# Kernel optimization log

Hardware: AMD Instinct MI355X
Metric: run time of the kernel (lower is better)

Reference implementation:

```python
import jax, jax.numpy as jnp
import numpy as np

N_H_NODES = 100000
N_G_NODES = 100000
N_EDGES = 1000000
N_GRAPHS = 64
N_H, N_G, N_X, N_U = 64, 64, 8, 16
IN_DIM = N_H + N_G + N_X + N_U  # 152
N_X_OUT = 1


def setup_inputs() -> dict:
    key = jax.random.key(0)
    ks = jax.random.split(key, 10)
    return {
        "x_h": jax.random.normal(ks[0], (N_H_NODES, N_H), dtype=jnp.float32),
        "x_g": jax.random.normal(ks[1], (N_G_NODES, N_G), dtype=jnp.float32),
        "edge_attr": jax.random.normal(ks[2], (N_EDGES, N_X), dtype=jnp.float32),
        "u": jax.random.normal(ks[3], (N_GRAPHS, N_U), dtype=jnp.float32),
        "edge_index": jax.random.randint(ks[4], (2, N_EDGES), 0, N_H_NODES, dtype=jnp.int64),
        "batch_e": jax.random.randint(ks[5], (N_EDGES,), 0, N_GRAPHS, dtype=jnp.int64),
        "W1": jax.random.normal(ks[6], (IN_DIM, N_X_OUT), dtype=jnp.float32) * 0.08,
        "b1": jnp.zeros((N_X_OUT,), dtype=jnp.float32),
        "W2": jax.random.normal(ks[7], (N_X_OUT, N_X_OUT), dtype=jnp.float32) * 0.5,
        "b2": jnp.zeros((N_X_OUT,), dtype=jnp.float32),
    }


def reference(x_h, x_g, edge_attr, u, edge_index, batch_e, W1, b1, W2, b2):
    src = edge_index[0]
    tgt = edge_index[1]
    # gather node/global features per edge and concat: [E, n_h+n_g+n_x+n_u]
    feat = jnp.concatenate([x_h[src], x_g[tgt], edge_attr, u[batch_e]], axis=1)
    h = feat @ W1 + b1                       # [E, 1]
    h = jnp.where(h >= 0, h, 0.1 * h)        # LeakyReLU(0.1)
    out = h @ W2 + b2                        # [E, 1]
    return out
```

## Files before the change

kernel.cpp:

```cpp
#include <hip/hip_runtime.h>
#include <hip/hip_bf16.h>


__global__ void node_partial_dot(const float* __restrict__ xh,
                                 const float* __restrict__ xg,
                                 const float* __restrict__ W1,
                                 float* __restrict__ ph,
                                 float* __restrict__ pg,
                                 int nh, int ng) {
    int gid  = blockIdx.x * blockDim.x + threadIdx.x;
    int wave = gid >> 6;
    int lane = gid & 63;
    int row  = wave * 4 + (lane >> 4);
    int q    = lane & 15;
    int total = nh + ng;
    if (row >= total) return;

    const float* src;
    const float* w;
    if (row < nh) { src = xh + (size_t)row * 64;        w = W1; }
    else          { src = xg + (size_t)(row - nh) * 64; w = W1 + 64; }

    float4 v  = reinterpret_cast<const float4*>(src)[q];
    float4 wv = reinterpret_cast<const float4*>(w)[q];
    float s = v.x * wv.x + v.y * wv.y + v.z * wv.z + v.w * wv.w;

    s += __shfl_xor(s, 1);
    s += __shfl_xor(s, 2);
    s += __shfl_xor(s, 4);
    s += __shfl_xor(s, 8);

    if (q == 0) {
        if (row < nh) ph[row] = s;
        else          pg[row - nh] = s;
    }
}

__global__ void edge_kernel(const int* __restrict__ edge_index,
                            const int* __restrict__ batch_e,
                            const float* __restrict__ edge_attr,
                            const float* __restrict__ u,
                            const float* __restrict__ W1,
                            const float* __restrict__ b1,
                            const float* __restrict__ W2,
                            const float* __restrict__ b2,
                            const float* __restrict__ ph,
                            const float* __restrict__ pg,
                            float* __restrict__ out,
                            int E) {
    int e = blockIdx.x * blockDim.x + threadIdx.x;
    if (e >= E) return;

    int s = edge_index[e];
    int t = edge_index[E + e];
    int g = batch_e[e];

    float h = ph[s] + pg[t] + b1[0];

    const float4* ea = reinterpret_cast<const float4*>(edge_attr + (size_t)e * 8);
    float4 a0 = ea[0], a1 = ea[1];
    const float* wx = W1 + 128;
    h += a0.x * wx[0] + a0.y * wx[1] + a0.z * wx[2] + a0.w * wx[3]
       + a1.x * wx[4] + a1.y * wx[5] + a1.z * wx[6] + a1.w * wx[7];

    const float4* ug  = reinterpret_cast<const float4*>(u + (size_t)g * 16);
    const float4* wu4 = reinterpret_cast<const float4*>(W1 + 136);
#pragma unroll
    for (int j = 0; j < 4; ++j) {
        float4 uv = ug[j];
        float4 wv = wu4[j];
        h += uv.x * wv.x + uv.y * wv.y + uv.z * wv.z + uv.w * wv.w;
    }

    h = (h >= 0.0f) ? h : 0.1f * h;
    out[e] = h * W2[0] + b2[0];
}

__global__ void edge_fallback(const int* __restrict__ edge_index,
                              const int* __restrict__ batch_e,
                              const float* __restrict__ xh,
                              const float* __restrict__ xg,
                              const float* __restrict__ edge_attr,
                              const float* __restrict__ u,
                              const float* __restrict__ W1,
                              const float* __restrict__ b1,
                              const float* __restrict__ W2,
                              const float* __restrict__ b2,
                              float* __restrict__ out,
                              int E) {
    int e = blockIdx.x * blockDim.x + threadIdx.x;
    if (e >= E) return;
    int s = edge_index[e];
    int t = edge_index[E + e];
    int g = batch_e[e];
    float h = b1[0];
    const float* hs = xh + (size_t)s * 64;
    const float* gt = xg + (size_t)t * 64;
#pragma unroll 8
    for (int j = 0; j < 64; ++j) h += hs[j] * W1[j];
#pragma unroll 8
    for (int j = 0; j < 64; ++j) h += gt[j] * W1[64 + j];
    const float* ea = edge_attr + (size_t)e * 8;
#pragma unroll
    for (int j = 0; j < 8; ++j) h += ea[j] * W1[128 + j];
    const float* ug = u + (size_t)g * 16;
#pragma unroll
    for (int j = 0; j < 16; ++j) h += ug[j] * W1[136 + j];
    h = (h >= 0.0f) ? h : 0.1f * h;
    out[e] = h * W2[0] + b2[0];
}

extern "C" void kernel_launch(void* const* d_in, const int* in_sizes, int n_in,
                              void* d_out, int out_size, void* d_ws, size_t ws_size,
                              hipStream_t stream) {
    const float* x_h       = (const float*)d_in[0];
    const float* x_g       = (const float*)d_in[1];
    const float* edge_attr = (const float*)d_in[2];
    const float* u         = (const float*)d_in[3];
    const int*   edge_idx  = (const int*)d_in[4];
    const int*   batch_e   = (const int*)d_in[5];
    const float* W1        = (const float*)d_in[6];
    const float* b1        = (const float*)d_in[7];
    const float* W2        = (const float*)d_in[8];
    const float* b2        = (const float*)d_in[9];
    float* out = (float*)d_out;

    const int E  = in_sizes[5];
    const int nh = in_sizes[0] / 64;
    const int ng = in_sizes[1] / 64;

    size_t need = (size_t)(nh + ng) * sizeof(float);
    if (ws_size >= need) {
        float* ph = (float*)d_ws;
        float* pg = ph + nh;
        int totalRows = nh + ng;
        int rowsPerBlock = 16;
        int nb = (totalRows + rowsPerBlock - 1) / rowsPerBlock;
        node_partial_dot<<<nb, 256, 0, stream>>>(x_h, x_g, W1, ph, pg, nh, ng);

        int eb = (E + 255) / 256;
        edge_kernel<<<eb, 256, 0, stream>>>(edge_idx, batch_e, edge_attr, u,
                                            W1, b1, W2, b2, ph, pg, out, E);
    } else {
        int eb = (E + 255) / 256;
        edge_fallback<<<eb, 256, 0, stream>>>(edge_idx, batch_e, x_h, x_g, edge_attr, u,
                                              W1, b1, W2, b2, out, E);
    }
}
```

Before: 31.11 us.

## Precompute per-graph u·W1 partials and process four edges per thread

The node precompute kernel also computes u[g]·W1 plus b1 for each graph, so the edge kernel gathers one scalar per edge instead of a 16-float row of u. The edge kernel now handles four edges per thread, using int4 index loads, eight float4 loads of edge_attr, and one float4 store. This cuts per-edge gather traffic and raises memory-level parallelism. In exchange there are fewer threads in flight and higher register use per thread.

After: 31.77 us. 2.1% more time.

```diff
diff --git a/kernel.cpp b/kernel.cpp
--- a/kernel.cpp
+++ b/kernel.cpp
@@ -2,78 +2,111 @@
 #include <hip/hip_bf16.h>
 
 
-__global__ void node_partial_dot(const float* __restrict__ xh,
-                                 const float* __restrict__ xg,
-                                 const float* __restrict__ W1,
-                                 float* __restrict__ ph,
-                                 float* __restrict__ pg,
-                                 int nh, int ng) {
-    int gid  = blockIdx.x * blockDim.x + threadIdx.x;
-    int wave = gid >> 6;
-    int lane = gid & 63;
-    int row  = wave * 4 + (lane >> 4);
-    int q    = lane & 15;
-    int total = nh + ng;
+__global__ void precompute_partials(const float* __restrict__ xh,
+                                    const float* __restrict__ xg,
+                                    const float* __restrict__ u,
+                                    const float* __restrict__ W1,
+                                    const float* __restrict__ b1,
+                                    float* __restrict__ ph,
+                                    float* __restrict__ pg,
+                                    float* __restrict__ pu,
+                                    int nh, int ng, int ngr) {
+    int gid = blockIdx.x * blockDim.x + threadIdx.x;
+    int row = gid >> 4;
+    int q   = gid & 15;
+    int total = nh + ng + ngr;
     if (row >= total) return;
 
-    const float* src;
-    const float* w;
-    if (row < nh) { src = xh + (size_t)row * 64;        w = W1; }
-    else          { src = xg + (size_t)(row - nh) * 64; w = W1 + 64; }
-
-    float4 v  = reinterpret_cast<const float4*>(src)[q];
-    float4 wv = reinterpret_cast<const float4*>(w)[q];
-    float s = v.x * wv.x + v.y * wv.y + v.z * wv.z + v.w * wv.w;
-
-    s += __shfl_xor(s, 1);
-    s += __shfl_xor(s, 2);
-    s += __shfl_xor(s, 4);
-    s += __shfl_xor(s, 8);
-
-    if (q == 0) {
-        if (row < nh) ph[row] = s;
-        else          pg[row - nh] = s;
+    if (row < nh + ng) {
+        const float* src = (row < nh) ? xh + (size_t)row * 64
+                                      : xg + (size_t)(row - nh) * 64;
+        const float* w   = (row < nh) ? W1 : W1 + 64;
+        float4 v  = reinterpret_cast<const float4*>(src)[q];
+        float4 wv = reinterpret_cast<const float4*>(w)[q];
+        float s = v.x * wv.x + v.y * wv.y + v.z * wv.z + v.w * wv.w;
+        s += __shfl_xor(s, 1);
+        s += __shfl_xor(s, 2);
+        s += __shfl_xor(s, 4);
+        s += __shfl_xor(s, 8);
+        if (q == 0) {
+            if (row < nh) ph[row] = s;
+            else          pg[row - nh] = s;
+        }
+    } else {
+        int g = row - nh - ng;
+        float s = 0.0f;
+        if (q < 4) {
+            float4 v  = reinterpret_cast<const float4*>(u + (size_t)g * 16)[q];
+            float4 wv = reinterpret_cast<const float4*>(W1 + 136)[q];
+            s = v.x * wv.x + v.y * wv.y + v.z * wv.z + v.w * wv.w;
+        }
+        s += __shfl_xor(s, 1);
+        s += __shfl_xor(s, 2);
+        if (q == 0) pu[g] = s + b1[0];
     }
 }
 
-__global__ void edge_kernel(const int* __restrict__ edge_index,
-                            const int* __restrict__ batch_e,
-                            const float* __restrict__ edge_attr,
-                            const float* __restrict__ u,
-                            const float* __restrict__ W1,
-                            const float* __restrict__ b1,
-                            const float* __restrict__ W2,
-                            const float* __restrict__ b2,
-                            const float* __restrict__ ph,
-                            const float* __restrict__ pg,
-                            float* __restrict__ out,
-                            int E) {
-    int e = blockIdx.x * blockDim.x + threadIdx.x;
-    if (e >= E) return;
+__global__ void edge_kernel4(const int* __restrict__ edge_index,
+                             const int* __restrict__ batch_e,
+                             const float* __restrict__ edge_attr,
+                             const float* __restrict__ W1,
+                             const float* __restrict__ W2,
+                             const float* __restrict__ b2,
+                             const float* __restrict__ ph,
+                             const float* __restrict__ pg,
+                             const float* __restrict__ pu,
+                             float* __restrict__ out,
+                             int E) {
+    int t = blockIdx.x * blockDim.x + threadIdx.x;
+    int base = t * 4;
+    if (base >= E) return;
 
-    int s = edge_index[e];
-    int t = edge_index[E + e];
-    int g = batch_e[e];
+    const float* wx = W1 + 128;
+    float w0 = wx[0], w1 = wx[1], w2 = wx[2], w3 = wx[3];
+    float w4 = wx[4], w5 = wx[5], w6 = wx[6], w7 = wx[7];
+    float w2s = W2[0], b2s = b2[0];
 
-    float h = ph[s] + pg[t] + b1[0];
+    if (base + 3 < E) {
+        int4 sv = *reinterpret_cast<const int4*>(edge_index + base);
+        int4 tv = *reinterpret_cast<const int4*>(edge_index + E + base);
+        int4 gv = *reinterpret_cast<const int4*>(batch_e + base);
 
-    const float4* ea = reinterpret_cast<const float4*>(edge_attr + (size_t)e * 8);
-    float4 a0 = ea[0], a1 = ea[1];
-    const float* wx = W1 + 128;
-    h += a0.x * wx[0] + a0.y * wx[1] + a0.z * wx[2] + a0.w * wx[3]
-       + a1.x * wx[4] + a1.y * wx[5] + a1.z * wx[6] + a1.w * wx[7];
+        const float4* eap = reinterpret_cast<const float4*>(edge_attr + (size_t)base * 8);
+        float4 ea[8];
+#pragma unroll
+        for (int j = 0; j < 8; ++j) ea[j] = eap[j];
 
-    const float4* ug  = reinterpret_cast<const float4*>(u + (size_t)g * 16);
-    const float4* wu4 = reinterpret_cast<const float4*>(W1 + 136);
+        float p0 = ph[sv.x], p1 = ph[sv.y], p2 = ph[sv.z], p3 = ph[sv.w];
+        float q0 = pg[tv.x], q1 = pg[tv.y], q2 = pg[tv.z], q3 = pg[tv.w];
+        float r0 = pu[gv.x], r1 = pu[gv.y], r2 = pu[gv.z], r3 = pu[gv.w];
+
+        float hv[4];
+        float pp[4] = {p0, p1, p2, p3};
+        float qq[4] = {q0, q1, q2, q3};
+        float rr[4] = {r0, r1, r2, r3};
 #pragma unroll
-    for (int j = 0; j < 4; ++j) {
-        float4 uv = ug[j];
-        float4 wv = wu4[j];
-        h += uv.x * wv.x + uv.y * wv.y + uv.z * wv.z + uv.w * wv.w;
+        for (int i = 0; i < 4; ++i) {
+            float4 a0 = ea[2 * i], a1 = ea[2 * i + 1];
+            float h = pp[i] + qq[i] + rr[i]
+                    + a0.x * w0 + a0.y * w1 + a0.z * w2 + a0.w * w3
+                    + a1.x * w4 + a1.y * w5 + a1.z * w6 + a1.w * w7;
+            h = (h >= 0.0f) ? h : 0.1f * h;
+            hv[i] = h * w2s + b2s;
+        }
+        *reinterpret_cast<float4*>(out + base) = make_float4(hv[0], hv[1], hv[2], hv[3]);
+    } else {
+        for (int e = base; e < E; ++e) {
+            int s = edge_index[e];
+            int tg = edge_index[E + e];
+            int g = batch_e[e];
+            const float* a = edge_attr + (size_t)e * 8;
+            float h = ph[s] + pg[tg] + pu[g]
+                    + a[0] * w0 + a[1] * w1 + a[2] * w2 + a[3] * w3
+                    + a[4] * w4 + a[5] * w5 + a[6] * w6 + a[7] * w7;
+            h = (h >= 0.0f) ? h : 0.1f * h;
+            out[e] = h * w2s + b2s;
+        }
     }
-
-    h = (h >= 0.0f) ? h : 0.1f * h;
-    out[e] = h * W2[0] + b2[0];
 }
 
 __global__ void edge_fallback(const int* __restrict__ edge_index,
@@ -125,22 +158,27 @@
     const float* b2        = (const float*)d_in[9];
     float* out = (float*)d_out;
 
-    const int E  = in_sizes[5];
-    const int nh = in_sizes[0] / 64;
-    const int ng = in_sizes[1] / 64;
+    const int E   = in_sizes[5];
+    const int nh  = in_sizes[0] / 64;
+    const int ng  = in_sizes[1] / 64;
+    const int ngr = in_sizes[3] / 16;
 
-    size_t need = (size_t)(nh + ng) * sizeof(float);
+    size_t need = (size_t)(nh + ng + ngr) * sizeof(float);
     if (ws_size >= need) {
         float* ph = (float*)d_ws;
         float* pg = ph + nh;
-        int totalRows = nh + ng;
+        float* pu = pg + ng;
+
+        int totalRows = nh + ng + ngr;
         int rowsPerBlock = 16;
         int nb = (totalRows + rowsPerBlock - 1) / rowsPerBlock;
-        node_partial_dot<<<nb, 256, 0, stream>>>(x_h, x_g, W1, ph, pg, nh, ng);
+        precompute_partials<<<nb, 256, 0, stream>>>(x_h, x_g, u, W1, b1,
+                                                    ph, pg, pu, nh, ng, ngr);
 
-        int eb = (E + 255) / 256;
-        edge_kernel<<<eb, 256, 0, stream>>>(edge_idx, batch_e, edge_attr, u,
-                                            W1, b1, W2, b2, ph, pg, out, E);
+        int threads = (E + 3) / 4;
+        int eb = (threads + 255) / 256;
+        edge_kernel4<<<eb, 256, 0, stream>>>(edge_idx, batch_e, edge_attr,
+                                             W1, W2, b2, ph, pg, pu, out, E);
     } else {
         int eb = (E + 255) / 256;
         edge_fallback<<<eb, 256, 0, stream>>>(edge_idx, batch_e, x_h, x_g, edge_attr, u,
```
